# Kernel tuning notes

Measured on AMD Instinct MI355X. Metric: run time of the kernel, lower is better.

## Reference

```python
import jax, jax.numpy as jnp
import numpy as np

D_MODEL, HEADS, D_K = 512, 8, 64
MIN_SPREAD, MIN_RBF, MAX_RBF = 2.0, 0.001, 1.0
NEG_INF = float('-inf')


def setup_inputs() -> dict:
    key = jax.random.key(0)
    ks = jax.random.split(key, 12)
    B, N = 2, 2048
    xav = (6.0 / (D_K + D_MODEL)) ** 0.5
    unif = lambda k, shape: jax.random.uniform(k, shape, jnp.float32, -xav, xav)
    return {
        'q': jax.random.normal(ks[0], (B, N, D_MODEL), jnp.float32),
        'k': jax.random.normal(ks[1], (B, N, D_MODEL), jnp.float32),
        'v': jax.random.normal(ks[2], (B, N, D_MODEL), jnp.float32),
        'coords': jax.random.normal(ks[3], (B, N, 3), jnp.float32),
        'mask': jnp.zeros((B, N), dtype=bool),
        'spread_weights': jnp.zeros((HEADS,), jnp.float32),
        'beta_weights': jnp.zeros((HEADS,), jnp.float32),
        'q_proj': unif(ks[4], (HEADS, D_MODEL, D_K)),
        'k_proj': unif(ks[5], (HEADS, D_MODEL, D_K)),
        'v_proj': unif(ks[6], (HEADS, D_MODEL, D_K)),
        'q_bias': jnp.zeros((HEADS, D_K), jnp.float32),
        'k_bias': jnp.zeros((HEADS, D_K), jnp.float32),
        'v_bias': jnp.zeros((HEADS, D_K), jnp.float32),
        'w_out': jax.random.normal(ks[7], (D_MODEL, D_MODEL), jnp.float32) * (1.0 / D_MODEL ** 0.5),
    }


def reference(q, k, v, coords, mask, spread_weights, beta_weights,
              q_proj, k_proj, v_proj, q_bias, k_bias, v_bias, w_out):
    B, N, _ = q.shape
    # per-head projections: [B,H,N,dk]
    Q = jnp.einsum('bnd,hdk->bhnk', q, q_proj) + q_bias[None, :, None, :]
    K = jnp.einsum('bnd,hdk->bhnk', k, k_proj) + k_bias[None, :, None, :]
    V = jnp.einsum('bnd,hdk->bhnk', v, v_proj) + v_bias[None, :, None, :]
    # scaled dot-product scores [B,H,N,N]
    S = jnp.einsum('bhnk,bhmk->bhnm', Q, K) / (D_K ** 0.5)
    # squared pairwise distances [B,N,N] (D = sqrt(D2); RBF uses -D^2 = -D2)
    D2 = jnp.sum((coords[:, :, None, :] - coords[:, None, :, :]) ** 2, axis=-1)
    spreads = MIN_SPREAD + jnp.exp(spread_weights)  # [H]
    betas = jnp.exp(beta_weights)                   # [H]
    R = jnp.exp(-D2[:, None, :, :] / (2.0 * spreads[None, :, None, None] ** 2))
    R_norm = 2.0 * (R - MIN_RBF) / (MAX_RBF - MIN_RBF) - 1.0
    SR = S + jnp.abs(S) * betas[None, :, None, None] * R_norm
    SR = jnp.where(mask[:, None, None, :], NEG_INF, SR)  # eval mode: drop_p = 0
    P = jax.nn.softmax(SR, axis=-1)
    out = jnp.einsum('bhnm,bhmk->bhnk', P, V)  # [B,H,N,dk]
    # permute(0,2,3,1) -> [B,N,dk,H], reshape to [B,N,d_model]
    out = jnp.transpose(out, (0, 2, 3, 1)).reshape(B, N, D_MODEL)
    return out @ w_out.T
```

## Files before the change

### kernel.cpp

```cpp
#include <hip/hip_runtime.h>
#include <hip/hip_fp16.h>

typedef unsigned short u16;
typedef __attribute__((ext_vector_type(4))) float f32x4;
typedef __attribute__((ext_vector_type(8))) short s16x8;

#define B_SZ 2
#define N_SZ 2048
#define H_SZ 8
#define DK 64
#define DM 512

static __device__ inline void mfma_f16(f32x4& acc, s16x8 a, s16x8 b) {
    asm volatile("v_mfma_f32_16x16x32_f16 %0, %1, %2, %0" : "+v"(acc) : "v"(a), "v"(b));
}
static __device__ inline u16 f16_rn(float f) { return __half_as_ushort(__float2half(f)); }

static __device__ inline s16x8 cvt8(const float4& a, const float4& b) {
    s16x8 r;
    r[0] = (short)f16_rn(a.x); r[1] = (short)f16_rn(a.y);
    r[2] = (short)f16_rn(a.z); r[3] = (short)f16_rn(a.w);
    r[4] = (short)f16_rn(b.x); r[5] = (short)f16_rn(b.y);
    r[6] = (short)f16_rn(b.z); r[7] = (short)f16_rn(b.w);
    return r;
}

static __device__ inline u16* swz(u16* base, int row, int byteoff) {
    return (u16*)((char*)base + row * 128 + (byteoff ^ ((row & 7) << 4)));
}
static __device__ inline const u16* swzc(const u16* base, int row, int byteoff) {
    return (const u16*)((const char*)base + row * 128 + (byteoff ^ ((row & 7) << 4)));
}

#if __has_builtin(__builtin_amdgcn_global_load_lds)
#define HAS_GLL 1
static __device__ inline void gll16(const u16* g, u16* l) {
    __builtin_amdgcn_global_load_lds(
        (const __attribute__((address_space(1))) unsigned int*)g,
        (__attribute__((address_space(3))) unsigned int*)l, 16, 0, 0);
}
#endif

static __device__ inline void stage16(const u16* gp, u16* lbase, int lane) {
#ifdef HAS_GLL
    gll16(gp, lbase);
#else
    *(s16x8*)(lbase + lane * 8) = *(const s16x8*)(gp);
#endif
}

__global__ void __launch_bounds__(256) k_prep(
    const float* __restrict__ q, const float* __restrict__ k,
    const float* __restrict__ v, const float* __restrict__ qp,
    const float* __restrict__ kp, const float* __restrict__ vp,
    const float* __restrict__ wo,
    u16* __restrict__ Pt, u16* __restrict__ Wb, u16* __restrict__ Af) {
    int blk = blockIdx.x, t = threadIdx.x;
    __shared__ float lds[64 * 65];
    if (blk < 192) {
        int z = blk >> 6, rem = blk & 63, h = rem >> 3, ddt = rem & 7;
        const float* src = (z == 0 ? qp : (z == 1 ? kp : vp)) + (size_t)h * DM * DK;
        u16* dst = Pt + ((size_t)(z * H_SZ + h)) * DK * DM;
#pragma unroll
        for (int i = 0; i < 16; i++) {
            int idx = i * 256 + t;
            int rr = idx >> 6, cc = idx & 63;
            lds[cc * 65 + rr] = src[(size_t)(ddt * 64 + rr) * DK + cc];
        }
        __syncthreads();
#pragma unroll
        for (int i = 0; i < 16; i++) {
            int idx = i * 256 + t;
            int kk = idx >> 6, dd = idx & 63;
            dst[(size_t)kk * DM + ddt * 64 + dd] = f16_rn(lds[kk * 65 + dd]);
        }
    } else if (blk < 448) {
        int i = (blk - 192) * 1024 + t * 4;
        float4 f = *(const float4*)(wo + i);
        ushort4 r;
        r.x = f16_rn(f.x); r.y = f16_rn(f.y); r.z = f16_rn(f.z); r.w = f16_rn(f.w);
        *(ushort4*)(Wb + i) = r;
    } else {
        size_t base = (size_t)(blk - 448) * 2048 + (size_t)t * 8;
        int z = (int)(base >> 21);
        size_t off = base & 2097151;
        const float* s = (z == 0 ? q : (z == 1 ? k : v)) + off;
        float4 f0 = *(const float4*)(s);
        float4 f1 = *(const float4*)(s + 4);
        *(s16x8*)(Af + base) = cvt8(f0, f1);
    }
}

__global__ void __launch_bounds__(256) k_proj_gemm(
    const u16* __restrict__ Af, const u16* __restrict__ Pt,
    const float* __restrict__ qbias, const float* __restrict__ kbias,
    const float* __restrict__ vbias,
    u16* __restrict__ Qb, u16* __restrict__ Kb, u16* __restrict__ Vt) {
    int z = blockIdx.z;
    const u16* A = Af + (size_t)z * (4096 * 512);
    const float* bias = z == 0 ? qbias : (z == 1 ? kbias : vbias);
    const u16* Bw = Pt + (size_t)z * (512 * 512);
    int m0 = blockIdx.x * 128, c0 = blockIdx.y * 64;
    int t = threadIdx.x, w = t >> 6, l = t & 63, g = (l >> 4), cl = l & 15;
    __shared__ __align__(16) u16 a_lds[128 * 64];
    f32x4 acc[2][4] = {};
    int srow_b = w * 8 + (l >> 3), schk = l & 7;
    for (int ks = 0; ks < 8; ks++) {
        __syncthreads();
#pragma unroll
        for (int cc = 0; cc < 4; cc++) {
            int row = cc * 32 + srow_b;
            const u16* gp = A + (size_t)(m0 + row) * 512 + ks * 64 + ((schk ^ (row & 7)) << 3);
            stage16(gp, a_lds + cc * 2048 + w * 512, l);
        }
        s16x8 bfrag[4][2];
#pragma unroll
        for (int st = 0; st < 4; st++) {
            int c = c0 + st * 16 + cl;
#pragma unroll
            for (int kk = 0; kk < 2; kk++)
                bfrag[st][kk] = *(const s16x8*)(Bw + (size_t)c * 512 + ks * 64 + kk * 32 + 8 * g);
        }
        __syncthreads();
#pragma unroll
        for (int rs = 0; rs < 2; rs++) {
            int row = w * 32 + rs * 16 + cl;
#pragma unroll
            for (int kk = 0; kk < 2; kk++) {
                s16x8 afrag = *(const s16x8*)swzc(a_lds, row, kk * 64 + 16 * g);
#pragma unroll
                for (int st = 0; st < 4; st++) mfma_f16(acc[rs][st], afrag, bfrag[st][kk]);
            }
        }
    }
    float sc = (z == 0) ? 0.125f : 1.0f;
#pragma unroll
    for (int rs = 0; rs < 2; rs++) {
#pragma unroll
        for (int st = 0; st < 4; st++) {
            int c = c0 + st * 16 + cl;
            int h = c >> 6, kk = c & 63;
            float bv = bias[c];
#pragma unroll
            for (int r = 0; r < 4; r++) {
                int m = m0 + w * 32 + rs * 16 + 4 * g + r;
                int b = m >> 11, n = m & 2047;
                u16 o = f16_rn((acc[rs][st][r] + bv) * sc);
                if (z == 2) {
                    Vt[((size_t)((b * H_SZ + h) * 32 + (n >> 6))) * 4096 + kk * 64 + (n & 63)] = o;
                } else {
                    u16* dst = (z == 0) ? Qb : Kb;
                    dst[((size_t)(b * H_SZ + h) * N_SZ + n) * DK + kk] = o;
                }
            }
        }
    }
}

__global__ void __launch_bounds__(512, 4) k_attn(
    const u16* __restrict__ Qb, const u16* __restrict__ Kb,
    const u16* __restrict__ Vt, const float* __restrict__ coords,
    const unsigned char* __restrict__ maskp,
    const float* __restrict__ spread_w, const float* __restrict__ beta_w,
    u16* __restrict__ Om) {
    int bid = blockIdx.x;
    int wid = (bid & 7) * 64 + (bid >> 3);
    int qt = wid & 31, bh = wid >> 5;
    int h = bh & 7, b = bh >> 3;
    int n0 = qt * 64;
    int t = threadIdx.x, w = t >> 6, l = t & 63, g = (l >> 4), cl = l & 15;
    int wq = w & 3, half = w >> 2;
    __shared__ __align__(16) u16 kbuf[2][4096];
    __shared__ __align__(16) u16 vbuf[2][4096];
    __shared__ __align__(16) u16 pbuf[8][1024];
    __shared__ float cjs[2][64][4];
    __shared__ unsigned char msks[2][64];

    int qrow = n0 + wq * 16 + cl;
    const u16* qp = Qb + ((size_t)bh * N_SZ + qrow) * DK;
    s16x8 qf0 = *(const s16x8*)(qp + 8 * g);
    s16x8 qf1 = *(const s16x8*)(qp + 32 + 8 * g);

    float qcx[4], qcy[4], qcz[4];
#pragma unroll
    for (int r = 0; r < 4; r++) {
        int row = n0 + wq * 16 + 4 * g + r;
        const float* cp = coords + ((size_t)b * N_SZ + row) * 3;
        qcx[r] = cp[0]; qcy[r] = cp[1]; qcz[r] = cp[2];
    }
    float sigma = 2.0f + __expf(spread_w[h]);
    float ninv = -1.0f / (2.0f * sigma * sigma);
    float beta = __expf(beta_w[h]);

    float mrun[4] = {-1e30f, -1e30f, -1e30f, -1e30f};
    float lsum[4] = {0.f, 0.f, 0.f, 0.f};
    f32x4 oacc[4] = {};
    int sid = t & 255, shalf = t >> 8, srow = sid >> 2, sq = sid & 3;
    const u16* kbase = Kb + (size_t)bh * N_SZ * DK;
    const u16* vbase = Vt + (size_t)bh * 32 * 4096;

    for (int it = 0; it < 16; it++) {
        int jts = it * 2 + shalf, j0s = jts * 64;
        __syncthreads();
        {
            const u16* ksrc = kbase + (size_t)(j0s + srow) * 64 + sq * 16;
            *(s16x8*)swz(kbuf[shalf], srow, sq * 32)      = *(const s16x8*)(ksrc);
            *(s16x8*)swz(kbuf[shalf], srow, sq * 32 + 16) = *(const s16x8*)(ksrc + 8);
            const u16* vsrc = vbase + (size_t)jts * 4096 + srow * 64 + sq * 16;
            *(s16x8*)swz(vbuf[shalf], srow, sq * 32)      = *(const s16x8*)(vsrc);
            *(s16x8*)swz(vbuf[shalf], srow, sq * 32 + 16) = *(const s16x8*)(vsrc + 8);
            if (sid < 64) {
                const float* cp = coords + ((size_t)b * N_SZ + j0s + sid) * 3;
                cjs[shalf][sid][0] = cp[0];
                cjs[shalf][sid][1] = cp[1];
                cjs[shalf][sid][2] = cp[2];
                msks[shalf][sid] = maskp[b * N_SZ + j0s + sid];
            }
        }
        __syncthreads();

        f32x4 s[4];
#pragma unroll
        for (int st = 0; st < 4; st++) {
            int jj = st * 16 + cl;
            s16x8 kf0 = *(const s16x8*)swzc(kbuf[half], jj, 16 * g);
            s16x8 kf1 = *(const s16x8*)swzc(kbuf[half], jj, 64 + 16 * g);
            f32x4 a = {};
            mfma_f16(a, qf0, kf0);
            mfma_f16(a, qf1, kf1);
            s[st] = a;
        }
        float sr[4][4];
#pragma unroll
        for (int st = 0; st < 4; st++) {
            int jj = st * 16 + cl;
            float cx = cjs[half][jj][0], cy = cjs[half][jj][1], cz = cjs[half][jj][2];
            bool mk = msks[half][jj] != 0;
#pragma unroll
            for (int r = 0; r < 4; r++) {
                float sv = s[st][r];
                float dx = qcx[r] - cx, dy = qcy[r] - cy, dz = qcz[r] - cz;
                float d2 = fmaf(dx, dx, fmaf(dy, dy, dz * dz));
                float rb = __expf(d2 * ninv);
                float rn = fmaf(2.002002f, rb, -1.002002f);
                sv = fmaf(fabsf(sv) * beta, rn, sv);
                sr[st][r] = mk ? -1e30f : sv;
            }
        }
        float tmx[4]; int need = 0;
#pragma unroll
        for (int r = 0; r < 4; r++) {
            float tm = fmaxf(fmaxf(sr[0][r], sr[1][r]), fmaxf(sr[2][r], sr[3][r]));
            tm = fmaxf(tm, __shfl_xor(tm, 1));
            tm = fmaxf(tm, __shfl_xor(tm, 2));
            tm = fmaxf(tm, __shfl_xor(tm, 4));
            tm = fmaxf(tm, __shfl_xor(tm, 8));
            tmx[r] = tm;
            if (tm > mrun[r] + 8.0f) need = 1;
        }
        if (__any(need)) {
#pragma unroll
            for (int r = 0; r < 4; r++) {
                float mn = fmaxf(mrun[r], tmx[r]);
                float corr = __expf(mrun[r] - mn);
                mrun[r] = mn;
                lsum[r] *= corr;
#pragma unroll
                for (int dst = 0; dst < 4; dst++) oacc[dst][r] *= corr;
            }
        }
#pragma unroll
        for (int st = 0; st < 4; st++) {
#pragma unroll
            for (int r = 0; r < 4; r++) {
                float p = __expf(sr[st][r] - mrun[r]);
                lsum[r] += p;
                int row = 4 * g + r;
                *swz(pbuf[w], row, (st * 16 + cl) * 2) = f16_rn(p);
            }
        }
#pragma unroll
        for (int kstep = 0; kstep < 2; kstep++) {
            s16x8 pf = *(const s16x8*)swzc(pbuf[w], cl, kstep * 64 + 16 * g);
#pragma unroll
            for (int dst = 0; dst < 4; dst++) {
                s16x8 vf = *(const s16x8*)swzc(vbuf[half], dst * 16 + cl, kstep * 64 + 16 * g);
                mfma_f16(oacc[dst], pf, vf);
            }
        }
    }
#pragma unroll
    for (int r = 0; r < 4; r++) {
        float s = lsum[r];
        s += __shfl_xor(s, 1); s += __shfl_xor(s, 2);
        s += __shfl_xor(s, 4); s += __shfl_xor(s, 8);
        lsum[r] = s;
    }
    __syncthreads();
    float* scrO = (float*)(&kbuf[0][0]);
    float* scrM = (float*)(&vbuf[0][0]);
    if (half == 1) {
#pragma unroll
        for (int r = 0; r < 4; r++) {
            int rr = 4 * g + r;
#pragma unroll
            for (int dst = 0; dst < 4; dst++)
                scrO[wq * 1024 + rr * 64 + dst * 16 + cl] = oacc[dst][r];
            if (cl == 0) {
                scrM[wq * 32 + rr] = mrun[r];
                scrM[wq * 32 + 16 + rr] = lsum[r];
            }
        }
    }
    __syncthreads();
    if (half == 0) {
#pragma unroll
        for (int r = 0; r < 4; r++) {
            int rr = 4 * g + r;
            float mu = scrM[wq * 32 + rr], lu = scrM[wq * 32 + 16 + rr];
            float M = fmaxf(mrun[r], mu);
            float pa = __expf(mrun[r] - M), pb = __expf(mu - M);
            float inv = 1.0f / (pa * lsum[r] + pb * lu);
            int row = n0 + wq * 16 + rr;
#pragma unroll
            for (int dst = 0; dst < 4; dst++) {
                float o = (pa * oacc[dst][r] + pb * scrO[wq * 1024 + rr * 64 + dst * 16 + cl]) * inv;
                Om[((size_t)b * N_SZ + row) * DM + (dst * 16 + cl) * 8 + h] = f16_rn(o);
            }
        }
    }
}

__global__ void __launch_bounds__(256) k_out_gemm(
    const u16* __restrict__ Om, const u16* __restrict__ Wb,
    float* __restrict__ out) {
    int m0 = blockIdx.x * 64, c0 = blockIdx.y * 64;
    int t = threadIdx.x, w = t >> 6, l = t & 63, g = (l >> 4), cl = l & 15;
    __shared__ __align__(16) u16 a_lds[64 * 64];
    f32x4 acc[4] = {};
    int srow_b = w * 8 + (l >> 3), schk = l & 7;
    for (int ks = 0; ks < 8; ks++) {
        __syncthreads();
#pragma unroll
        for (int cc = 0; cc < 2; cc++) {
            int row = cc * 32 + srow_b;
            const u16* gp = Om + (size_t)(m0 + row) * 512 + ks * 64 + ((schk ^ (row & 7)) << 3);
            stage16(gp, a_lds + cc * 2048 + w * 512, l);
        }
        s16x8 bfrag[4][2];
#pragma unroll
        for (int st = 0; st < 4; st++) {
            int c = c0 + st * 16 + cl;
#pragma unroll
            for (int kk = 0; kk < 2; kk++)
                bfrag[st][kk] = *(const s16x8*)(Wb + (size_t)c * 512 + ks * 64 + kk * 32 + 8 * g);
        }
        __syncthreads();
        int row = w * 16 + cl;
#pragma unroll
        for (int kk = 0; kk < 2; kk++) {
            s16x8 afrag = *(const s16x8*)swzc(a_lds, row, kk * 64 + 16 * g);
#pragma unroll
            for (int st = 0; st < 4; st++) mfma_f16(acc[st], afrag, bfrag[st][kk]);
        }
    }
#pragma unroll
    for (int st = 0; st < 4; st++) {
        int c = c0 + st * 16 + cl;
#pragma unroll
        for (int r = 0; r < 4; r++) {
            int m = m0 + w * 16 + 4 * g + r;
            out[(size_t)m * 512 + c] = acc[st][r];
        }
    }
}

extern "C" void kernel_launch(void* const* d_in, const int* in_sizes, int n_in,
                              void* d_out, int out_size, void* d_ws, size_t ws_size,
                              hipStream_t stream) {
    const float* q      = (const float*)d_in[0];
    const float* k      = (const float*)d_in[1];
    const float* v      = (const float*)d_in[2];
    const float* coords = (const float*)d_in[3];
    const unsigned char* mask = (const unsigned char*)d_in[4];
    const float* sw     = (const float*)d_in[5];
    const float* bw     = (const float*)d_in[6];
    const float* qp     = (const float*)d_in[7];
    const float* kp     = (const float*)d_in[8];
    const float* vp     = (const float*)d_in[9];
    const float* qbias  = (const float*)d_in[10];
    const float* kbias  = (const float*)d_in[11];
    const float* vbias  = (const float*)d_in[12];
    const float* wo     = (const float*)d_in[13];

    char* ws = (char*)d_ws;
    u16* Pt = (u16*)(ws);
    u16* Wb = (u16*)(ws + 1572864);
    u16* Af = (u16*)(ws + 2097152);
    u16* Qb = (u16*)(ws + 14680064);
    u16* Kb = (u16*)(ws + 18874368);
    u16* Vt = (u16*)(ws + 23068672);
    u16* Om = (u16*)(ws + 27262976);

    k_prep<<<dim3(3520), 256, 0, stream>>>(q, k, v, qp, kp, vp, wo, Pt, Wb, Af);
    k_proj_gemm<<<dim3(32, 8, 3), 256, 0, stream>>>(Af, Pt, qbias, kbias, vbias, Qb, Kb, Vt);
    k_attn<<<dim3(512), 512, 0, stream>>>(Qb, Kb, Vt, coords, mask, sw, bw, Om);
    k_out_gemm<<<dim3(64, 8), 256, 0, stream>>>(Om, Wb, (float*)d_out);
}
```

Before: 215.9 us.

## Restructure attention into split-K warps with direct global loads and exp2 math

```diff
diff --git a/kernel.cpp b/kernel.cpp
--- a/kernel.cpp
+++ b/kernel.cpp
@@ -2,19 +2,31 @@
 #include <hip/hip_fp16.h>
 
 typedef unsigned short u16;
+typedef unsigned int u32;
 typedef __attribute__((ext_vector_type(4))) float f32x4;
 typedef __attribute__((ext_vector_type(8))) short s16x8;
+typedef __attribute__((ext_vector_type(2))) unsigned int u32x2;
+typedef __fp16 fp16x2 __attribute__((ext_vector_type(2)));
 
 #define B_SZ 2
 #define N_SZ 2048
 #define H_SZ 8
 #define DK 64
 #define DM 512
+#define QSC 0.18033688f
 
 static __device__ inline void mfma_f16(f32x4& acc, s16x8 a, s16x8 b) {
     asm volatile("v_mfma_f32_16x16x32_f16 %0, %1, %2, %0" : "+v"(acc) : "v"(a), "v"(b));
 }
 static __device__ inline u16 f16_rn(float f) { return __half_as_ushort(__float2half(f)); }
+
+static __device__ inline u32 pkrtz(float a, float b) {
+    union { fp16x2 h; u32 u; } cv;
+    cv.h = __builtin_amdgcn_cvt_pkrtz(a, b);
+    return cv.u;
+}
+
+#define EXP2(x) exp2f(x)
 
 static __device__ inline s16x8 cvt8(const float4& a, const float4& b) {
     s16x8 r;
@@ -25,9 +37,6 @@
     return r;
 }
 
-static __device__ inline u16* swz(u16* base, int row, int byteoff) {
-    return (u16*)((char*)base + row * 128 + (byteoff ^ ((row & 7) << 4)));
-}
 static __device__ inline const u16* swzc(const u16* base, int row, int byteoff) {
     return (const u16*)((const char*)base + row * 128 + (byteoff ^ ((row & 7) << 4)));
 }
@@ -40,7 +49,6 @@
         (__attribute__((address_space(3))) unsigned int*)l, 16, 0, 0);
 }
 #endif
-
 static __device__ inline void stage16(const u16* gp, u16* lbase, int lane) {
 #ifdef HAS_GLL
     gll16(gp, lbase);
@@ -53,14 +61,17 @@
     const float* __restrict__ q, const float* __restrict__ k,
     const float* __restrict__ v, const float* __restrict__ qp,
     const float* __restrict__ kp, const float* __restrict__ vp,
-    const float* __restrict__ wo,
-    u16* __restrict__ Pt, u16* __restrict__ Wb, u16* __restrict__ Af) {
+    const float* __restrict__ wo, const float* __restrict__ coords,
+    const unsigned char* __restrict__ maskp,
+    u16* __restrict__ Pt, u16* __restrict__ Wb2, u16* __restrict__ Af,
+    float4* __restrict__ C4, float* __restrict__ mbias) {
     int blk = blockIdx.x, t = threadIdx.x;
     __shared__ float lds[64 * 65];
     if (blk < 192) {
         int z = blk >> 6, rem = blk & 63, h = rem >> 3, ddt = rem & 7;
         const float* src = (z == 0 ? qp : (z == 1 ? kp : vp)) + (size_t)h * DM * DK;
         u16* dst = Pt + ((size_t)(z * H_SZ + h)) * DK * DM;
+        float sc = (z == 0) ? QSC : 1.0f;
 #pragma unroll
         for (int i = 0; i < 16; i++) {
             int idx = i * 256 + t;
@@ -72,22 +83,31 @@
         for (int i = 0; i < 16; i++) {
             int idx = i * 256 + t;
             int kk = idx >> 6, dd = idx & 63;
-            dst[(size_t)kk * DM + ddt * 64 + dd] = f16_rn(lds[kk * 65 + dd]);
-        }
-    } else if (blk < 448) {
-        int i = (blk - 192) * 1024 + t * 4;
-        float4 f = *(const float4*)(wo + i);
-        ushort4 r;
-        r.x = f16_rn(f.x); r.y = f16_rn(f.y); r.z = f16_rn(f.z); r.w = f16_rn(f.w);
-        *(ushort4*)(Wb + i) = r;
-    } else {
-        size_t base = (size_t)(blk - 448) * 2048 + (size_t)t * 8;
+            dst[(size_t)kk * DM + ddt * 64 + dd] = f16_rn(lds[kk * 65 + dd] * sc);
+        }
+    } else if (blk < 320) {
+        int idx8 = (blk - 192) * 256 + t;
+        int base = idx8 * 8;
+        int c = base >> 9, col0 = base & 511;
+        int h = col0 >> 6, d0 = col0 & 63;
+        s16x8 r;
+#pragma unroll
+        for (int i = 0; i < 8; i++)
+            r[i] = (short)f16_rn(wo[(size_t)c * 512 + (d0 + i) * 8 + h]);
+        *(s16x8*)(Wb2 + base) = r;
+    } else if (blk < 3392) {
+        size_t base = (size_t)(blk - 320) * 2048 + (size_t)t * 8;
         int z = (int)(base >> 21);
         size_t off = base & 2097151;
         const float* s = (z == 0 ? q : (z == 1 ? k : v)) + off;
         float4 f0 = *(const float4*)(s);
         float4 f1 = *(const float4*)(s + 4);
         *(s16x8*)(Af + base) = cvt8(f0, f1);
+    } else {
+        int i = (blk - 3392) * 256 + t;
+        float x = coords[(size_t)i * 3], y = coords[(size_t)i * 3 + 1], z = coords[(size_t)i * 3 + 2];
+        C4[i] = make_float4(x, y, z, x * x + y * y + z * z);
+        mbias[i] = maskp[i] ? -1e30f : 0.0f;
     }
 }
 
@@ -102,17 +122,25 @@
     const u16* Bw = Pt + (size_t)z * (512 * 512);
     int m0 = blockIdx.x * 128, c0 = blockIdx.y * 64;
     int t = threadIdx.x, w = t >> 6, l = t & 63, g = (l >> 4), cl = l & 15;
-    __shared__ __align__(16) u16 a_lds[128 * 64];
+    __shared__ __align__(16) u16 a_lds[2][128 * 64];
     f32x4 acc[2][4] = {};
     int srow_b = w * 8 + (l >> 3), schk = l & 7;
+
+#define STAGE_P(ks, buf)                                                              \
+    {                                                                                 \
+        _Pragma("unroll") for (int cc = 0; cc < 4; cc++) {                            \
+            int row = cc * 32 + srow_b;                                               \
+            const u16* gp = A + (size_t)(m0 + row) * 512 + (ks) * 64 +                \
+                            ((schk ^ (row & 7)) << 3);                                \
+            stage16(gp, a_lds[buf] + cc * 2048 + w * 512, l);                         \
+        }                                                                             \
+    }
+
+    STAGE_P(0, 0);
     for (int ks = 0; ks < 8; ks++) {
+        int cur = ks & 1;
         __syncthreads();
-#pragma unroll
-        for (int cc = 0; cc < 4; cc++) {
-            int row = cc * 32 + srow_b;
-            const u16* gp = A + (size_t)(m0 + row) * 512 + ks * 64 + ((schk ^ (row & 7)) << 3);
-            stage16(gp, a_lds + cc * 2048 + w * 512, l);
-        }
+        if (ks < 7) STAGE_P(ks + 1, cur ^ 1);
         s16x8 bfrag[4][2];
 #pragma unroll
         for (int st = 0; st < 4; st++) {
@@ -121,133 +149,153 @@
             for (int kk = 0; kk < 2; kk++)
                 bfrag[st][kk] = *(const s16x8*)(Bw + (size_t)c * 512 + ks * 64 + kk * 32 + 8 * g);
         }
-        __syncthreads();
 #pragma unroll
         for (int rs = 0; rs < 2; rs++) {
             int row = w * 32 + rs * 16 + cl;
 #pragma unroll
             for (int kk = 0; kk < 2; kk++) {
-                s16x8 afrag = *(const s16x8*)swzc(a_lds, row, kk * 64 + 16 * g);
+                s16x8 afrag = *(const s16x8*)swzc(a_lds[cur], row, kk * 64 + 16 * g);
 #pragma unroll
                 for (int st = 0; st < 4; st++) mfma_f16(acc[rs][st], afrag, bfrag[st][kk]);
             }
         }
     }
-    float sc = (z == 0) ? 0.125f : 1.0f;
-#pragma unroll
-    for (int rs = 0; rs < 2; rs++) {
-#pragma unroll
-        for (int st = 0; st < 4; st++) {
-            int c = c0 + st * 16 + cl;
-            int h = c >> 6, kk = c & 63;
-            float bv = bias[c];
-#pragma unroll
-            for (int r = 0; r < 4; r++) {
-                int m = m0 + w * 32 + rs * 16 + 4 * g + r;
-                int b = m >> 11, n = m & 2047;
-                u16 o = f16_rn((acc[rs][st][r] + bv) * sc);
-                if (z == 2) {
-                    Vt[((size_t)((b * H_SZ + h) * 32 + (n >> 6))) * 4096 + kk * 64 + (n & 63)] = o;
-                } else {
-                    u16* dst = (z == 0) ? Qb : Kb;
-                    dst[((size_t)(b * H_SZ + h) * N_SZ + n) * DK + kk] = o;
+#undef STAGE_P
+
+    if (z == 2) {
+        int h = blockIdx.y;
+        int b = m0 >> 11;
+        u16* vl = a_lds[0];
+        __syncthreads();
+#pragma unroll
+        for (int rs = 0; rs < 2; rs++) {
+#pragma unroll
+            for (int st = 0; st < 4; st++) {
+                int d = st * 16 + cl;
+                float bv = bias[c0 + st * 16 + cl];
+#pragma unroll
+                for (int r = 0; r < 4; r++) {
+                    int row = w * 32 + rs * 16 + 4 * g + r;
+                    int jt = row >> 6, jl = row & 63;
+                    int jp = (jl & 15) * 4 + (jl >> 4);
+                    vl[jt * 4096 + d * 64 + jp] = f16_rn(acc[rs][st][r] + bv);
                 }
             }
         }
-    }
-}
-
-__global__ void __launch_bounds__(512, 4) k_attn(
+        __syncthreads();
+        int jt = t >> 7, rem = t & 127, d = rem >> 1, qh = t & 1;
+        const u16* src = vl + jt * 4096 + d * 64 + qh * 32;
+        int jtile = ((m0 & 2047) >> 6) + jt;
+        u16* dst = Vt + ((size_t)((b * H_SZ + h) * 32 + jtile)) * 4096 + d * 64 + qh * 32;
+        *(s16x8*)(dst) = *(const s16x8*)(src);
+        *(s16x8*)(dst + 8) = *(const s16x8*)(src + 8);
+        *(s16x8*)(dst + 16) = *(const s16x8*)(src + 16);
+        *(s16x8*)(dst + 24) = *(const s16x8*)(src + 24);
+    } else {
+        float bsc = (z == 0) ? QSC : 1.0f;
+        u16* dst = (z == 0) ? Qb : Kb;
+#pragma unroll
+        for (int rs = 0; rs < 2; rs++) {
+#pragma unroll
+            for (int st = 0; st < 4; st++) {
+                int c = c0 + st * 16 + cl;
+                int h = c >> 6, kk = c & 63;
+                float bv = bias[c] * bsc;
+#pragma unroll
+                for (int r = 0; r < 4; r++) {
+                    int m = m0 + w * 32 + rs * 16 + 4 * g + r;
+                    int b = m >> 11, n = m & 2047;
+                    dst[((size_t)(b * H_SZ + h) * N_SZ + n) * DK + kk] = f16_rn(acc[rs][st][r] + bv);
+                }
+            }
+        }
+    }
+}
+
+__global__ void __launch_bounds__(256, 4) k_attn(
     const u16* __restrict__ Qb, const u16* __restrict__ Kb,
-    const u16* __restrict__ Vt, const float* __restrict__ coords,
-    const unsigned char* __restrict__ maskp,
+    const u16* __restrict__ Vt, const float4* __restrict__ C4,
+    const float* __restrict__ mbias,
     const float* __restrict__ spread_w, const float* __restrict__ beta_w,
     u16* __restrict__ Om) {
     int bid = blockIdx.x;
-    int wid = (bid & 7) * 64 + (bid >> 3);
-    int qt = wid & 31, bh = wid >> 5;
+    int wid = (bid & 7) * 256 + (bid >> 3);
+    int qg = wid & 127, bh = wid >> 7;
     int h = bh & 7, b = bh >> 3;
-    int n0 = qt * 64;
-    int t = threadIdx.x, w = t >> 6, l = t & 63, g = (l >> 4), cl = l & 15;
-    int wq = w & 3, half = w >> 2;
-    __shared__ __align__(16) u16 kbuf[2][4096];
-    __shared__ __align__(16) u16 vbuf[2][4096];
-    __shared__ __align__(16) u16 pbuf[8][1024];
-    __shared__ float cjs[2][64][4];
-    __shared__ unsigned char msks[2][64];
-
-    int qrow = n0 + wq * 16 + cl;
-    const u16* qp = Qb + ((size_t)bh * N_SZ + qrow) * DK;
+    int n0 = qg * 16;
+    int t = threadIdx.x, w = t >> 6, l = t & 63, g = l >> 4, cl = l & 15;
+
+    __shared__ __align__(16) float smem[4 * 16 * 64];
+    __shared__ float mergeML[4][2][16];
+    u16* pbufW = (u16*)smem + w * 1024;
+
+    const u16* qp = Qb + ((size_t)bh * N_SZ + n0 + cl) * DK;
     s16x8 qf0 = *(const s16x8*)(qp + 8 * g);
     s16x8 qf1 = *(const s16x8*)(qp + 32 + 8 * g);
 
-    float qcx[4], qcy[4], qcz[4];
+    float sigma = 2.0f + __expf(spread_w[h]);
+    float ninv2 = -0.72134752f / (sigma * sigma);
+    float beta = __expf(beta_w[h]);
+    float rnA = 2.002002f * beta, rnB = -1.002002f * beta;
+    float m2n = -2.0f * ninv2;
+
+    float qx2[4], qy2[4], qz2[4], aR[4];
 #pragma unroll
     for (int r = 0; r < 4; r++) {
-        int row = n0 + wq * 16 + 4 * g + r;
-        const float* cp = coords + ((size_t)b * N_SZ + row) * 3;
-        qcx[r] = cp[0]; qcy[r] = cp[1]; qcz[r] = cp[2];
-    }
-    float sigma = 2.0f + __expf(spread_w[h]);
-    float ninv = -1.0f / (2.0f * sigma * sigma);
-    float beta = __expf(beta_w[h]);
+        float4 c4 = C4[b * N_SZ + n0 + 4 * g + r];
+        qx2[r] = c4.x * m2n; qy2[r] = c4.y * m2n; qz2[r] = c4.z * m2n;
+        aR[r] = ninv2 * c4.w;
+    }
 
     float mrun[4] = {-1e30f, -1e30f, -1e30f, -1e30f};
     float lsum[4] = {0.f, 0.f, 0.f, 0.f};
     f32x4 oacc[4] = {};
-    int sid = t & 255, shalf = t >> 8, srow = sid >> 2, sq = sid & 3;
-    const u16* kbase = Kb + (size_t)bh * N_SZ * DK;
-    const u16* vbase = Vt + (size_t)bh * 32 * 4096;
-
-    for (int it = 0; it < 16; it++) {
-        int jts = it * 2 + shalf, j0s = jts * 64;
-        __syncthreads();
-        {
-            const u16* ksrc = kbase + (size_t)(j0s + srow) * 64 + sq * 16;
-            *(s16x8*)swz(kbuf[shalf], srow, sq * 32)      = *(const s16x8*)(ksrc);
-            *(s16x8*)swz(kbuf[shalf], srow, sq * 32 + 16) = *(const s16x8*)(ksrc + 8);
-            const u16* vsrc = vbase + (size_t)jts * 4096 + srow * 64 + sq * 16;
-            *(s16x8*)swz(vbuf[shalf], srow, sq * 32)      = *(const s16x8*)(vsrc);
-            *(s16x8*)swz(vbuf[shalf], srow, sq * 32 + 16) = *(const s16x8*)(vsrc + 8);
-            if (sid < 64) {
-                const float* cp = coords + ((size_t)b * N_SZ + j0s + sid) * 3;
-                cjs[shalf][sid][0] = cp[0];
-                cjs[shalf][sid][1] = cp[1];
-                cjs[shalf][sid][2] = cp[2];
-                msks[shalf][sid] = maskp[b * N_SZ + j0s + sid];
-            }
-        }
-        __syncthreads();
-
+
+    const u16* kTile = Kb + (size_t)bh * N_SZ * DK;
+    const u16* vTile = Vt + (size_t)bh * 32 * 4096;
+    const float4* c4b = C4 + b * N_SZ;
+    const float* mbb = mbias + b * N_SZ;
+
+    for (int jt = w; jt < 32; jt += 4) {
+        int j0 = jt * 64;
+        s16x8 kf[4][2];
+#pragma unroll
+        for (int st = 0; st < 4; st++) {
+            const u16* kr = kTile + (size_t)(j0 + st * 16 + cl) * DK + 8 * g;
+            kf[st][0] = *(const s16x8*)(kr);
+            kf[st][1] = *(const s16x8*)(kr + 32);
+        }
+        float cxv[4], cyv[4], czv[4], bJ[4], mb[4];
+#pragma unroll
+        for (int st = 0; st < 4; st++) {
+            float4 cc = c4b[j0 + st * 16 + cl];
+            cxv[st] = cc.x; cyv[st] = cc.y; czv[st] = cc.z;
+            bJ[st] = ninv2 * cc.w;
+            mb[st] = mbb[j0 + st * 16 + cl];
+        }
         f32x4 s[4];
 #pragma unroll
         for (int st = 0; st < 4; st++) {
-            int jj = st * 16 + cl;
-            s16x8 kf0 = *(const s16x8*)swzc(kbuf[half], jj, 16 * g);
-            s16x8 kf1 = *(const s16x8*)swzc(kbuf[half], jj, 64 + 16 * g);
             f32x4 a = {};
-            mfma_f16(a, qf0, kf0);
-            mfma_f16(a, qf1, kf1);
+            mfma_f16(a, qf0, kf[st][0]);
+            mfma_f16(a, qf1, kf[st][1]);
             s[st] = a;
         }
         float sr[4][4];
 #pragma unroll
         for (int st = 0; st < 4; st++) {
-            int jj = st * 16 + cl;
-            float cx = cjs[half][jj][0], cy = cjs[half][jj][1], cz = cjs[half][jj][2];
-            bool mk = msks[half][jj] != 0;
 #pragma unroll
             for (int r = 0; r < 4; r++) {
+                float arg = fmaf(qx2[r], cxv[st],
+                            fmaf(qy2[r], cyv[st],
+                            fmaf(qz2[r], czv[st], aR[r] + bJ[st])));
+                float rb = EXP2(arg);
                 float sv = s[st][r];
-                float dx = qcx[r] - cx, dy = qcy[r] - cy, dz = qcz[r] - cz;
-                float d2 = fmaf(dx, dx, fmaf(dy, dy, dz * dz));
-                float rb = __expf(d2 * ninv);
-                float rn = fmaf(2.002002f, rb, -1.002002f);
-                sv = fmaf(fabsf(sv) * beta, rn, sv);
-                sr[st][r] = mk ? -1e30f : sv;
-            }
-        }
-        float tmx[4]; int need = 0;
+                sv = fmaf(fabsf(sv), fmaf(rnA, rb, rnB), sv);
+                sr[st][r] = sv + mb[st];
+            }
+        }
+        float tmx[4]; bool need = false;
 #pragma unroll
         for (int r = 0; r < 4; r++) {
             float tm = fmaxf(fmaxf(sr[0][r], sr[1][r]), fmaxf(sr[2][r], sr[3][r]));
@@ -256,13 +304,13 @@
             tm = fmaxf(tm, __shfl_xor(tm, 4));
             tm = fmaxf(tm, __shfl_xor(tm, 8));
             tmx[r] = tm;
-            if (tm > mrun[r] + 8.0f) need = 1;
+            need = need || (tm > mrun[r] + 8.0f);
         }
         if (__any(need)) {
 #pragma unroll
             for (int r = 0; r < 4; r++) {
                 float mn = fmaxf(mrun[r], tmx[r]);
-                float corr = __expf(mrun[r] - mn);
+                float corr = EXP2(mrun[r] - mn);
                 mrun[r] = mn;
                 lsum[r] *= corr;
 #pragma unroll
@@ -270,21 +318,22 @@
             }
         }
 #pragma unroll
-        for (int st = 0; st < 4; st++) {
-#pragma unroll
-            for (int r = 0; r < 4; r++) {
-                float p = __expf(sr[st][r] - mrun[r]);
-                lsum[r] += p;
-                int row = 4 * g + r;
-                *swz(pbuf[w], row, (st * 16 + cl) * 2) = f16_rn(p);
-            }
-        }
-#pragma unroll
-        for (int kstep = 0; kstep < 2; kstep++) {
-            s16x8 pf = *(const s16x8*)swzc(pbuf[w], cl, kstep * 64 + 16 * g);
+        for (int r = 0; r < 4; r++) {
+            float p0 = EXP2(sr[0][r] - mrun[r]);
+            float p1 = EXP2(sr[1][r] - mrun[r]);
+            float p2 = EXP2(sr[2][r] - mrun[r]);
+            float p3 = EXP2(sr[3][r] - mrun[r]);
+            lsum[r] += (p0 + p1) + (p2 + p3);
+            u32x2 pw = {pkrtz(p0, p1), pkrtz(p2, p3)};
+            *(u32x2*)&pbufW[(4 * g + r) * 64 + cl * 4] = pw;
+        }
+        const u16* vp_ = vTile + (size_t)jt * 4096;
+#pragma unroll
+        for (int ks = 0; ks < 2; ks++) {
+            s16x8 pf = *(const s16x8*)&pbufW[cl * 64 + ks * 32 + 8 * g];
 #pragma unroll
             for (int dst = 0; dst < 4; dst++) {
-                s16x8 vf = *(const s16x8*)swzc(vbuf[half], dst * 16 + cl, kstep * 64 + 16 * g);
+                s16x8 vf = *(const s16x8*)(vp_ + (size_t)(dst * 16 + cl) * 64 + ks * 32 + 8 * g);
                 mfma_f16(oacc[dst], pf, vf);
             }
         }
@@ -297,80 +346,88 @@
         lsum[r] = s;
     }
     __syncthreads();
-    float* scrO = (float*)(&kbuf[0][0]);
-    float* scrM = (float*)(&vbuf[0][0]);
-    if (half == 1) {
-#pragma unroll
-        for (int r = 0; r < 4; r++) {
-            int rr = 4 * g + r;
-#pragma unroll
-            for (int dst = 0; dst < 4; dst++)
-                scrO[wq * 1024 + rr * 64 + dst * 16 + cl] = oacc[dst][r];
-            if (cl == 0) {
-                scrM[wq * 32 + rr] = mrun[r];
-                scrM[wq * 32 + 16 + rr] = lsum[r];
-            }
+#pragma unroll
+    for (int r = 0; r < 4; r++) {
+        int row = 4 * g + r;
+#pragma unroll
+        for (int dst = 0; dst < 4; dst++)
+            smem[(w * 16 + row) * 64 + dst * 16 + cl] = oacc[dst][r];
+        if (cl == 0) {
+            mergeML[w][0][row] = mrun[r];
+            mergeML[w][1][row] = lsum[r];
         }
     }
     __syncthreads();
-    if (half == 0) {
-#pragma unroll
-        for (int r = 0; r < 4; r++) {
-            int rr = 4 * g + r;
-            float mu = scrM[wq * 32 + rr], lu = scrM[wq * 32 + 16 + rr];
-            float M = fmaxf(mrun[r], mu);
-            float pa = __expf(mrun[r] - M), pb = __expf(mu - M);
-            float inv = 1.0f / (pa * lsum[r] + pb * lu);
-            int row = n0 + wq * 16 + rr;
-#pragma unroll
-            for (int dst = 0; dst < 4; dst++) {
-                float o = (pa * oacc[dst][r] + pb * scrO[wq * 1024 + rr * 64 + dst * 16 + cl]) * inv;
-                Om[((size_t)b * N_SZ + row) * DM + (dst * 16 + cl) * 8 + h] = f16_rn(o);
-            }
-        }
+#pragma unroll
+    for (int rr = 0; rr < 4; rr++) {
+        int row = w * 4 + rr;
+        float m0_ = fmaxf(fmaxf(mergeML[0][0][row], mergeML[1][0][row]),
+                          fmaxf(mergeML[2][0][row], mergeML[3][0][row]));
+        float num = 0.f, den = 0.f;
+#pragma unroll
+        for (int js = 0; js < 4; js++) {
+            float e = EXP2(mergeML[js][0][row] - m0_);
+            num = fmaf(e, smem[(js * 16 + row) * 64 + l], num);
+            den = fmaf(e, mergeML[js][1][row], den);
+        }
+        Om[((size_t)b * N_SZ + n0 + row) * DM + h * 64 + l] = f16_rn(num / den);
     }
 }
 
 __global__ void __launch_bounds__(256) k_out_gemm(
-    const u16* __restrict__ Om, const u16* __restrict__ Wb,
+    const u16* __restrict__ Om, const u16* __restrict__ Wb2,
     float* __restrict__ out) {
-    int m0 = blockIdx.x * 64, c0 = blockIdx.y * 64;
+    int m0 = blockIdx.x * 128, c0 = blockIdx.y * 64;
     int t = threadIdx.x, w = t >> 6, l = t & 63, g = (l >> 4), cl = l & 15;
-    __shared__ __align__(16) u16 a_lds[64 * 64];
-    f32x4 acc[4] = {};
+    __shared__ __align__(16) u16 a_lds[2][128 * 64];
+    f32x4 acc[2][4] = {};
     int srow_b = w * 8 + (l >> 3), schk = l & 7;
+
+#define STAGE_O(ks, buf)                                                              \
+    {                                                                                 \
+        _Pragma("unroll") for (int cc = 0; cc < 4; cc++) {                            \
+            int row = cc * 32 + srow_b;                                               \
+            const u16* gp = Om + (size_t)(m0 + row) * 512 + (ks) * 64 +               \
+                            ((schk ^ (row & 7)) << 3);                                \
+            stage16(gp, a_lds[buf] + cc * 2048 + w * 512, l);                         \
+        }                                                                             \
+    }
+
+    STAGE_O(0, 0);
     for (int ks = 0; ks < 8; ks++) {
+        int cur = ks & 1;
         __syncthreads();
-#pragma unroll
-        for (int cc = 0; cc < 2; cc++) {
-            int row = cc * 32 + srow_b;
-            const u16* gp = Om + (size_t)(m0 + row) * 512 + ks * 64 + ((schk ^ (row & 7)) << 3);
-            stage16(gp, a_lds + cc * 2048 + w * 512, l);
-        }
+        if (ks < 7) STAGE_O(ks + 1, cur ^ 1);
         s16x8 bfrag[4][2];
 #pragma unroll
         for (int st = 0; st < 4; st++) {
             int c = c0 + st * 16 + cl;
 #pragma unroll
             for (int kk = 0; kk < 2; kk++)
-                bfrag[st][kk] = *(const s16x8*)(Wb + (size_t)c * 512 + ks * 64 + kk * 32 + 8 * g);
-        }
-        __syncthreads();
-        int row = w * 16 + cl;
-#pragma unroll
-        for (int kk = 0; kk < 2; kk++) {
-            s16x8 afrag = *(const s16x8*)swzc(a_lds, row, kk * 64 + 16 * g);
-#pragma unroll
-            for (int st = 0; st < 4; st++) mfma_f16(acc[st], afrag, bfrag[st][kk]);
-        }
-    }
-#pragma unroll
-    for (int st = 0; st < 4; st++) {
-        int c = c0 + st * 16 + cl;
-#pragma unroll
-        for (int r = 0; r < 4; r++) {
-            int m = m0 + w * 16 + 4 * g + r;
-            out[(size_t)m * 512 + c] = acc[st][r];
+                bfrag[st][kk] = *(const s16x8*)(Wb2 + (size_t)c * 512 + ks * 64 + kk * 32 + 8 * g);
+        }
+#pragma unroll
+        for (int rs = 0; rs < 2; rs++) {
+            int row = w * 32 + rs * 16 + cl;
+#pragma unroll
+            for (int kk = 0; kk < 2; kk++) {
+                s16x8 afrag = *(const s16x8*)swzc(a_lds[cur], row, kk * 64 + 16 * g);
+#pragma unroll
+                for (int st = 0; st < 4; st++) mfma_f16(acc[rs][st], afrag, bfrag[st][kk]);
+            }
+        }
+    }
+#undef STAGE_O
+#pragma unroll
+    for (int rs = 0; rs < 2; rs++) {
+#pragma unroll
+        for (int st = 0; st < 4; st++) {
+            int c = c0 + st * 16 + cl;
+#pragma unroll
+            for (int r = 0; r < 4; r++) {
+                int m = m0 + w * 32 + rs * 16 + 4 * g + r;
+                out[(size_t)m * 512 + c] = acc[rs][st][r];
+            }
         }
     }
 }
@@ -394,16 +451,19 @@
     const float* wo     = (const float*)d_in[13];
 
     char* ws = (char*)d_ws;
-    u16* Pt = (u16*)(ws);
-    u16* Wb = (u16*)(ws + 1572864);
-    u16* Af = (u16*)(ws + 2097152);
-    u16* Qb = (u16*)(ws + 14680064);
-    u16* Kb = (u16*)(ws + 18874368);
-    u16* Vt = (u16*)(ws + 23068672);
-    u16* Om = (u16*)(ws + 27262976);
-
-    k_prep<<<dim3(3520), 256, 0, stream>>>(q, k, v, qp, kp, vp, wo, Pt, Wb, Af);
+    u16*    Pt    = (u16*)(ws);
+    u16*    Wb2   = (u16*)(ws + 1572864);
+    u16*    Af    = (u16*)(ws + 2097152);
+    u16*    Qb    = (u16*)(ws + 14680064);
+    u16*    Kb    = (u16*)(ws + 18874368);
+    u16*    Vt    = (u16*)(ws + 23068672);
+    u16*    Om    = (u16*)(ws + 27262976);
+    float4* C4    = (float4*)(ws + 31457280);
+    float*  mbias = (float*)(ws + 31522816);
+
+    k_prep<<<dim3(3408), 256, 0, stream>>>(q, k, v, qp, kp, vp, wo, coords, mask,
+                                           Pt, Wb2, Af, C4, mbias);
     k_proj_gemm<<<dim3(32, 8, 3), 256, 0, stream>>>(Af, Pt, qbias, kbias, vbias, Qb, Kb, Vt);
-    k_attn<<<dim3(512), 512, 0, stream>>>(Qb, Kb, Vt, coords, mask, sw, bw, Om);
-    k_out_gemm<<<dim3(64, 8), 256, 0, stream>>>(Om, Wb, (float*)d_out);
-}
+    k_attn<<<dim3(2048), 256, 0, stream>>>(Qb, Kb, Vt, C4, mbias, sw, bw, Om);
+    k_out_gemm<<<dim3(32, 8), 256, 0, stream>>>(Om, Wb2, (float*)d_out);
+}
```

Result: slower. 288.0 us (+33.4%).
